# Kernel tuning notes

Measured on AMD Instinct MI355X. Metric: run time of the kernel, lower is better.

## Reference

```python
import jax, jax.numpy as jnp
import numpy as np

N_NODES = 50000
N_EDGES = 1600000
D = 128
L = 4
N_GRAPHS = 512


def setup_inputs() -> dict:
    key = jax.random.key(0)
    ks = jax.random.split(key, 8)
    x = jax.random.normal(ks[0], (N_NODES, D), dtype=jnp.float32)
    edge_index = jax.random.randint(ks[1], (2, N_EDGES), 0, N_NODES, dtype=jnp.int64)
    batch = jnp.sort(jax.random.randint(ks[2], (N_NODES,), 0, N_GRAPHS, dtype=jnp.int64))
    # MLP params per GIN layer: Linear(D->D), ReLU, Linear(D->D). Stacked over L layers.
    s = 1.0 / np.sqrt(D)
    Ws1 = jax.random.uniform(ks[3], (L, D, D), jnp.float32, -s, s)
    bs1 = jax.random.uniform(ks[4], (L, D), jnp.float32, -s, s)
    Ws2 = jax.random.uniform(ks[5], (L, D, D), jnp.float32, -s, s)
    bs2 = jax.random.uniform(ks[6], (L, D), jnp.float32, -s, s)
    return {"x": x, "edge_index": edge_index, "batch": batch,
            "Ws1": Ws1, "bs1": bs1, "Ws2": Ws2, "bs2": bs2}


def reference(x, edge_index, batch, Ws1, bs1, Ws2, bs2):
    src, dst = edge_index[0], edge_index[1]
    for l in range(L):
        # GINConv (eps=0): h = MLP(x + sum_{j in N(i)} x_j)
        agg = jax.ops.segment_sum(x[src], dst, num_segments=N_NODES)  # [N, D]
        h = x + agg
        h = jax.nn.relu(h @ Ws1[l] + bs1[l])
        x = h @ Ws2[l] + bs2[l]
    # global_add_pool: segment-sum node features by graph id
    return jax.ops.segment_sum(x, batch, num_segments=N_GRAPHS)  # [G, D]
```

## Files before the change

### kernel.cpp

```cpp
#include <hip/hip_runtime.h>

#define NN 50000
#define NE 1600000
#define DD 128
#define NL 4
#define NG 512
#define BSH 7
#define BMSK 127
#define NBUK 391
#define NBLK 196
#define EPB 8192
#define HN (NBUK * NBLK)
#define HT 150
#define EPT 20

typedef __attribute__((ext_vector_type(8))) short short8;
typedef __attribute__((ext_vector_type(4))) float floatx4;

__device__ __forceinline__ unsigned short f2bf(float f) {
    unsigned int u = __float_as_uint(f);
    u += 0x7fffu + ((u >> 16) & 1u);
    return (unsigned short)(u >> 16);
}
__device__ __forceinline__ float bf2f(unsigned short u) {
    return __uint_as_float(((unsigned int)u) << 16);
}

__global__ __launch_bounds__(256) void cvt_kernel(const float* __restrict__ x,
                                                  unsigned short* __restrict__ xbf) {
    int idx = blockIdx.x * 256 + threadIdx.x;
    float4 f = ((const float4*)x)[idx];
    ushort4 o;
    o.x = f2bf(f.x); o.y = f2bf(f.y); o.z = f2bf(f.z); o.w = f2bf(f.w);
    ((ushort4*)xbf)[idx] = o;
}


__global__ __launch_bounds__(512) void shist_kernel(const int* __restrict__ src,
                                                    int* __restrict__ hist) {
    __shared__ int h[NBUK];
    int tid = threadIdx.x;
    for (int i = tid; i < NBUK; i += 512) h[i] = 0;
    __syncthreads();
    int base = blockIdx.x * EPB;
#pragma unroll
    for (int it = 0; it < EPB / 512; it++) {
        int e = base + it * 512 + tid;
        if (e < NE) atomicAdd(&h[src[e] >> BSH], 1);
    }
    __syncthreads();
    for (int i = tid; i < NBUK; i += 512) hist[i * NBLK + blockIdx.x] = h[i];
}

__global__ __launch_bounds__(512) void sum_tiles_kernel(const int* __restrict__ in,
                                                        int* __restrict__ tsum, int n) {
    int i = blockIdx.x * 512 + threadIdx.x;
    __shared__ int s[512];
    s[threadIdx.x] = (i < n) ? in[i] : 0;
    __syncthreads();
    for (int off = 256; off > 0; off >>= 1) {
        if (threadIdx.x < off) s[threadIdx.x] += s[threadIdx.x + off];
        __syncthreads();
    }
    if (threadIdx.x == 0) tsum[blockIdx.x] = s[0];
}

__global__ __launch_bounds__(256) void scan_tiles_kernel(const int* __restrict__ tsum,
                                                         int* __restrict__ toff, int ntiles) {
    int t = threadIdx.x;
    __shared__ int s[256];
    int v = (t < ntiles) ? tsum[t] : 0;
    s[t] = v;
    __syncthreads();
    for (int off = 1; off < 256; off <<= 1) {
        int u = (t >= off) ? s[t - off] : 0;
        __syncthreads();
        s[t] += u;
        __syncthreads();
    }
    if (t < ntiles) toff[t] = s[t] - v;
}

__global__ __launch_bounds__(512) void scan_out_kernel(const int* __restrict__ in,
                                                       const int* __restrict__ toff,
                                                       int* __restrict__ out, int n) {
    int i = blockIdx.x * 512 + threadIdx.x;
    int t = threadIdx.x;
    int v = (i < n) ? in[i] : 0;
    __shared__ int s[512];
    s[t] = v;
    __syncthreads();
    for (int off = 1; off < 512; off <<= 1) {
        int u = (t >= off) ? s[t - off] : 0;
        __syncthreads();
        s[t] += u;
        __syncthreads();
    }
    if (i < n) out[i] = toff[blockIdx.x] + s[t] - v;
}

__global__ __launch_bounds__(512) void sscatter_kernel(const int* __restrict__ src,
                                                       const int* __restrict__ dst,
                                                       const int* __restrict__ soff,
                                                       unsigned int* __restrict__ ebufA) {
    __shared__ int h[NBUK];
    int tid = threadIdx.x;
    for (int i = tid; i < NBUK; i += 512) h[i] = 0;
    __syncthreads();
    int base = blockIdx.x * EPB;
#pragma unroll
    for (int it = 0; it < EPB / 512; it++) {
        int e = base + it * 512 + tid;
        if (e < NE) {
            int s = src[e];
            int ss = s >> BSH;
            int p = atomicAdd(&h[ss], 1);
            ebufA[soff[ss * NBLK + blockIdx.x] + p] =
                ((unsigned int)dst[e] << 16) | (unsigned int)s;
        }
    }
}

__global__ __launch_bounds__(512) void bhist_kernel(const unsigned int* __restrict__ ebufA,
                                                    int* __restrict__ hist) {
    __shared__ int h[NBUK];
    int tid = threadIdx.x;
    for (int i = tid; i < NBUK; i += 512) h[i] = 0;
    __syncthreads();
    int base = blockIdx.x * EPB;
#pragma unroll
    for (int it = 0; it < EPB / 512; it++) {
        int e = base + it * 512 + tid;
        if (e < NE) atomicAdd(&h[ebufA[e] >> (16 + BSH)], 1);
    }
    __syncthreads();
    for (int i = tid; i < NBUK; i += 512) hist[i * NBLK + blockIdx.x] = h[i];
}

__global__ __launch_bounds__(512) void bscatter_kernel(const unsigned int* __restrict__ ebufA,
                                                       const int* __restrict__ bkoff,
                                                       int* __restrict__ ebuf) {
    __shared__ int h[NBUK];
    int tid = threadIdx.x;
    for (int i = tid; i < NBUK; i += 512) h[i] = 0;
    __syncthreads();
    int base = blockIdx.x * EPB;
#pragma unroll
    for (int it = 0; it < EPB / 512; it++) {
        int e = base + it * 512 + tid;
        if (e < NE) {
            unsigned int pk = ebufA[e];
            int d = pk >> 16;
            int s = pk & 0xFFFF;
            int bu = d >> BSH;
            int p = atomicAdd(&h[bu], 1);
            ebuf[bkoff[bu * NBLK + blockIdx.x] + p] = (s << BSH) | (d & BMSK);
        }
    }
}

__global__ __launch_bounds__(256) void bucket_csr_kernel(const int* __restrict__ ebuf,
                                                         const int* __restrict__ bkoff,
                                                         int* __restrict__ rowptr,
                                                         int* __restrict__ rowend,
                                                         int* __restrict__ col) {
    __shared__ int cnt[128], exc[128], ebase[128];
    int b = blockIdx.x, tid = threadIdx.x;
    int segstart = bkoff[b * NBLK];
    int segend = (b < NBUK - 1) ? bkoff[(b + 1) * NBLK] : NE;
    if (tid < 128) cnt[tid] = 0;
    __syncthreads();
    int evr[EPT];
    int rnk[EPT];
#pragma unroll
    for (int j = 0; j < EPT; j++) {
        int i = segstart + tid + j * 256;
        if (i < segend) {
            int ev = ebuf[i];
            evr[j] = ev;
            rnk[j] = atomicAdd(&cnt[ev & BMSK], 1);
        } else {
            evr[j] = -1;
        }
    }
    __syncthreads();
    int v = (tid < 128) ? cnt[tid] : 0;
    if (tid < 128) exc[tid] = v;
    __syncthreads();
    for (int off = 1; off < 128; off <<= 1) {
        int u = (tid < 128 && tid >= off) ? exc[tid - off] : 0;
        __syncthreads();
        if (tid < 128) exc[tid] += u;
        __syncthreads();
    }
    if (tid < 128) {
        int excl = exc[tid] - v;
        ebase[tid] = segstart + excl;
        int node = (b << BSH) + tid;
        if (node < NN) {
            rowptr[node] = segstart + excl;
            rowend[node] = segstart + excl + v;
        }
    }
    __syncthreads();
#pragma unroll
    for (int j = 0; j < EPT; j++) {
        if (evr[j] >= 0) {
            int low = evr[j] & BMSK;
            col[ebase[low] + rnk[j]] = ((unsigned)evr[j]) >> BSH;
        }
    }
}

__global__ __launch_bounds__(256) void prep_kernel(const float* __restrict__ Ws1,
                                                   const float* __restrict__ Ws2,
                                                   unsigned short* __restrict__ W1T,
                                                   unsigned short* __restrict__ W2T) {
    int idx = blockIdx.x * 256 + threadIdx.x;
    int l = idx >> 14;
    int rem = idx & 16383;
    int k = rem >> 7;
    int n = rem & 127;
    int o = (l << 14) + (n << 7) + k;
    W1T[o] = f2bf(Ws1[idx]);
    W2T[o] = f2bf(Ws2[idx]);
}

__global__ __launch_bounds__(256) void agg_kernel(const unsigned short* __restrict__ xbf,
                                                  const int* __restrict__ rowptr,
                                                  const int* __restrict__ rowend,
                                                  const int* __restrict__ col,
                                                  unsigned short* __restrict__ hpre) {
    int g = threadIdx.x >> 4;
    int lane = threadIdx.x & 15;
    int node = blockIdx.x * 16 + g;
    const uint4* base = (const uint4*)xbf;
    float a[8];
    {
        uint4 v = base[node * 16 + lane];
        a[0] = __uint_as_float(v.x << 16); a[1] = __uint_as_float(v.x & 0xFFFF0000u);
        a[2] = __uint_as_float(v.y << 16); a[3] = __uint_as_float(v.y & 0xFFFF0000u);
        a[4] = __uint_as_float(v.z << 16); a[5] = __uint_as_float(v.z & 0xFFFF0000u);
        a[6] = __uint_as_float(v.w << 16); a[7] = __uint_as_float(v.w & 0xFFFF0000u);
    }
    int s = rowptr[node], e = rowend[node];
    int i = s;
    for (; i + 8 <= e; i += 8) {
        uint4 v0 = base[col[i] * 16 + lane];
        uint4 v1 = base[col[i + 1] * 16 + lane];
        uint4 v2 = base[col[i + 2] * 16 + lane];
        uint4 v3 = base[col[i + 3] * 16 + lane];
        uint4 v4 = base[col[i + 4] * 16 + lane];
        uint4 v5 = base[col[i + 5] * 16 + lane];
        uint4 v6 = base[col[i + 6] * 16 + lane];
        uint4 v7 = base[col[i + 7] * 16 + lane];
#define ACC(V)                                                            \
        a[0] += __uint_as_float(V.x << 16); a[1] += __uint_as_float(V.x & 0xFFFF0000u); \
        a[2] += __uint_as_float(V.y << 16); a[3] += __uint_as_float(V.y & 0xFFFF0000u); \
        a[4] += __uint_as_float(V.z << 16); a[5] += __uint_as_float(V.z & 0xFFFF0000u); \
        a[6] += __uint_as_float(V.w << 16); a[7] += __uint_as_float(V.w & 0xFFFF0000u)
        ACC(v0); ACC(v1); ACC(v2); ACC(v3); ACC(v4); ACC(v5); ACC(v6); ACC(v7);
    }
    for (; i < e; i++) {
        uint4 v = base[col[i] * 16 + lane];
        ACC(v);
    }
#undef ACC
    uint4 o;
    o.x = (unsigned int)f2bf(a[0]) | ((unsigned int)f2bf(a[1]) << 16);
    o.y = (unsigned int)f2bf(a[2]) | ((unsigned int)f2bf(a[3]) << 16);
    o.z = (unsigned int)f2bf(a[4]) | ((unsigned int)f2bf(a[5]) << 16);
    o.w = (unsigned int)f2bf(a[6]) | ((unsigned int)f2bf(a[7]) << 16);
    ((uint4*)hpre)[node * 16 + lane] = o;
}

__global__ __launch_bounds__(256) void mlp_kernel(const unsigned short* __restrict__ A,
                                                  const unsigned short* __restrict__ W1,
                                                  const float* __restrict__ b1,
                                                  const unsigned short* __restrict__ W2,
                                                  const float* __restrict__ b2,
                                                  unsigned short* __restrict__ O) {
    __shared__ unsigned short Wl[128 * 128];
    __shared__ unsigned short Hl[128 * 128];
    int tid = threadIdx.x;
    int wg = tid >> 6;
    int lane = tid & 63;
    int quad = lane >> 4;
    int li = lane & 15;
    int mg = wg >> 1, ng = wg & 1;
    int rowb = blockIdx.x * 128;

    {
        const uint4* wgl = (const uint4*)W1;
#pragma unroll
        for (int it = 0; it < 8; it++) {
            int idx = it * 256 + tid;
            int n = idx >> 4, kc = idx & 15;
            *(uint4*)&Wl[n * 128 + ((kc * 8) ^ ((n & 7) << 3))] = wgl[idx];
        }
    }
    __syncthreads();

    floatx4 acc[4][4];
#pragma unroll
    for (int tn = 0; tn < 4; tn++)
#pragma unroll
        for (int mi = 0; mi < 4; mi++) acc[tn][mi] = (floatx4){0.f, 0.f, 0.f, 0.f};

#pragma unroll
    for (int kk = 0; kk < 4; kk++) {
        int kc = kk * 32 + quad * 8;
        short8 xf[4];
#pragma unroll
        for (int mi = 0; mi < 4; mi++) {
            int ar = rowb + mg * 64 + mi * 16 + li;
            xf[mi] = (ar < NN) ? *(const short8*)(A + (size_t)ar * DD + kc)
                               : (short8){0, 0, 0, 0, 0, 0, 0, 0};
        }
#pragma unroll
        for (int tn = 0; tn < 4; tn++) {
            int wr = ng * 64 + tn * 16 + li;
            short8 wf = *(const short8*)&Wl[wr * 128 + (kc ^ ((wr & 7) << 3))];
#pragma unroll
            for (int mi = 0; mi < 4; mi++)
                acc[tn][mi] = __builtin_amdgcn_mfma_f32_16x16x32_bf16(wf, xf[mi], acc[tn][mi], 0, 0, 0);
        }
    }

#pragma unroll
    for (int tn = 0; tn < 4; tn++) {
        float4 bv = ((const float4*)b1)[ng * 16 + tn * 4 + quad];
#pragma unroll
        for (int mi = 0; mi < 4; mi++) {
            int hr = mg * 64 + mi * 16 + li;
            float v0 = fmaxf(acc[tn][mi][0] + bv.x, 0.f);
            float v1 = fmaxf(acc[tn][mi][1] + bv.y, 0.f);
            float v2 = fmaxf(acc[tn][mi][2] + bv.z, 0.f);
            float v3 = fmaxf(acc[tn][mi][3] + bv.w, 0.f);
            uint2 u;
            u.x = (unsigned int)f2bf(v0) | ((unsigned int)f2bf(v1) << 16);
            u.y = (unsigned int)f2bf(v2) | ((unsigned int)f2bf(v3) << 16);
            int c = (ng * 64 + tn * 16 + quad * 4) ^ ((hr & 7) << 3);
            *(uint2*)&Hl[hr * 128 + c] = u;
        }
    }
    __syncthreads();

    {
        const uint4* wgl = (const uint4*)W2;
#pragma unroll
        for (int it = 0; it < 8; it++) {
            int idx = it * 256 + tid;
            int n = idx >> 4, kc = idx & 15;
            *(uint4*)&Wl[n * 128 + ((kc * 8) ^ ((n & 7) << 3))] = wgl[idx];
        }
    }
    __syncthreads();

#pragma unroll
    for (int tn = 0; tn < 4; tn++)
#pragma unroll
        for (int mi = 0; mi < 4; mi++) acc[tn][mi] = (floatx4){0.f, 0.f, 0.f, 0.f};

#pragma unroll
    for (int kk = 0; kk < 4; kk++) {
        int kc = kk * 32 + quad * 8;
        short8 hf[4];
#pragma unroll
        for (int mi = 0; mi < 4; mi++) {
            int hr = mg * 64 + mi * 16 + li;
            hf[mi] = *(const short8*)&Hl[hr * 128 + (kc ^ ((hr & 7) << 3))];
        }
#pragma unroll
        for (int tn = 0; tn < 4; tn++) {
            int wr = ng * 64 + tn * 16 + li;
            short8 wf = *(const short8*)&Wl[wr * 128 + (kc ^ ((wr & 7) << 3))];
#pragma unroll
            for (int mi = 0; mi < 4; mi++)
                acc[tn][mi] = __builtin_amdgcn_mfma_f32_16x16x32_bf16(wf, hf[mi], acc[tn][mi], 0, 0, 0);
        }
    }

#pragma unroll
    for (int tn = 0; tn < 4; tn++) {
        float4 bv = ((const float4*)b2)[ng * 16 + tn * 4 + quad];
#pragma unroll
        for (int mi = 0; mi < 4; mi++) {
            int m = rowb + mg * 64 + mi * 16 + li;
            if (m < NN) {
                uint2 u;
                u.x = (unsigned int)f2bf(acc[tn][mi][0] + bv.x) |
                      ((unsigned int)f2bf(acc[tn][mi][1] + bv.y) << 16);
                u.y = (unsigned int)f2bf(acc[tn][mi][2] + bv.z) |
                      ((unsigned int)f2bf(acc[tn][mi][3] + bv.w) << 16);
                *(uint2*)&O[(size_t)m * DD + ng * 64 + tn * 16 + quad * 4] = u;
            }
        }
    }
}

__global__ __launch_bounds__(128) void pool_kernel(const unsigned short* __restrict__ x,
                                                   const int* __restrict__ batch,
                                                   float* __restrict__ out) {
    int g = blockIdx.x;
    int lo = 0, hi = NN;
    while (lo < hi) { int mid = (lo + hi) >> 1; if (batch[mid] < g) lo = mid + 1; else hi = mid; }
    int s = lo;
    hi = NN;
    while (lo < hi) { int mid = (lo + hi) >> 1; if (batch[mid] < g + 1) lo = mid + 1; else hi = mid; }
    int e = lo;
    int d = threadIdx.x;
    float acc = 0.f;
    for (int i = s; i < e; i++) acc += bf2f(x[(size_t)i * DD + d]);
    out[g * DD + d] = acc;
}

extern "C" void kernel_launch(void* const* d_in, const int* in_sizes, int n_in,
                              void* d_out, int out_size, void* d_ws, size_t ws_size,
                              hipStream_t stream) {
    const float* x0 = (const float*)d_in[0];
    const int* edge = (const int*)d_in[1];
    const int* batch = (const int*)d_in[2];
    const float* Ws1 = (const float*)d_in[3];
    const float* bs1 = (const float*)d_in[4];
    const float* Ws2 = (const float*)d_in[5];
    const float* bs2 = (const float*)d_in[6];
    float* out = (float*)d_out;
    const int* src = edge;
    const int* dst = edge + NE;

    char* ws = (char*)d_ws;
    size_t off = 0;
    auto alloc = [&](size_t bytes) {
        void* p = ws + off;
        off += (bytes + 255) & ~(size_t)255;
        return p;
    };
    unsigned short* x0bf = (unsigned short*)alloc((size_t)NN * DD * 2);
    unsigned short* xA = (unsigned short*)alloc((size_t)NN * DD * 2);
    unsigned short* xB = (unsigned short*)alloc((size_t)NN * DD * 2);
    unsigned short* hpre = (unsigned short*)alloc((size_t)NN * DD * 2);
    int* col = (int*)alloc((size_t)NE * 4);
    int* ebuf = (int*)alloc((size_t)NE * 4);
    unsigned int* ebufA = (unsigned int*)alloc((size_t)NE * 4);
    int* hist = (int*)alloc((size_t)HN * 4);
    int* bkoff = (int*)alloc((size_t)HN * 4);
    int* soff = (int*)alloc((size_t)HN * 4);
    int* tsum = (int*)alloc((size_t)HT * 4);
    int* toff = (int*)alloc((size_t)HT * 4);
    int* rowptr = (int*)alloc((size_t)(NN + 1) * 4);
    int* rowend = (int*)alloc((size_t)NN * 4);
    unsigned short* W1T = (unsigned short*)alloc((size_t)NL * DD * DD * 2);
    unsigned short* W2T = (unsigned short*)alloc((size_t)NL * DD * DD * 2);

    cvt_kernel<<<(NN * DD / 4) / 256, 256, 0, stream>>>(x0, x0bf);
    shist_kernel<<<NBLK, 512, 0, stream>>>(src, hist);
    sum_tiles_kernel<<<HT, 512, 0, stream>>>(hist, tsum, HN);
    scan_tiles_kernel<<<1, 256, 0, stream>>>(tsum, toff, HT);
    scan_out_kernel<<<HT, 512, 0, stream>>>(hist, toff, soff, HN);
    sscatter_kernel<<<NBLK, 512, 0, stream>>>(src, dst, soff, ebufA);
    bhist_kernel<<<NBLK, 512, 0, stream>>>(ebufA, hist);
    sum_tiles_kernel<<<HT, 512, 0, stream>>>(hist, tsum, HN);
    scan_tiles_kernel<<<1, 256, 0, stream>>>(tsum, toff, HT);
    scan_out_kernel<<<HT, 512, 0, stream>>>(hist, toff, bkoff, HN);
    bscatter_kernel<<<NBLK, 512, 0, stream>>>(ebufA, bkoff, ebuf);
    bucket_csr_kernel<<<NBUK, 256, 0, stream>>>(ebuf, bkoff, rowptr, rowend, col);
    prep_kernel<<<(NL * DD * DD) / 256, 256, 0, stream>>>(Ws1, Ws2, W1T, W2T);

    const unsigned short* xin = x0bf;
    unsigned short* bufs[2] = {xA, xB};
    const int mlp_grid = (NN + 127) / 128;
    for (int l = 0; l < NL; l++) {
        agg_kernel<<<NN / 16, 256, 0, stream>>>(xin, rowptr, rowend, col, hpre);
        unsigned short* xout = bufs[l & 1];
        mlp_kernel<<<mlp_grid, 256, 0, stream>>>(hpre, W1T + l * DD * DD, bs1 + l * DD,
                                                 W2T + l * DD * DD, bs2 + l * DD, xout);
        xin = xout;
    }
    pool_kernel<<<NG, 128, 0, stream>>>(xin, batch, out);
}
```

Measured before the change: 453.3 us.

## Fuse prelude kernels and replace three-pass scan with single-pass lookback scan

Merges the x conversion, weight transpose/convert and source histogram into one prelude kernel. Replaces each three-kernel scan (tile sums, tile scan, output scan) with a single-pass decoupled-lookback scan that uses per-tile status flags in global memory, which are reset by a memset. This cuts kernel launches and inter-kernel gaps in the CSR build. The lookback spin-waits rely on all 150 blocks being co-resident, and the memset adds one extra operation.

```diff
diff --git a/kernel.cpp b/kernel.cpp
--- a/kernel.cpp
+++ b/kernel.cpp
@@ -13,6 +13,8 @@
 #define HN (NBUK * NBLK)
 #define HT 150
 #define EPT 20
+#define CVT_N (NN * DD / 4)
+#define PREP_N (NL * DD * DD)
 
 typedef __attribute__((ext_vector_type(8))) short short8;
 typedef __attribute__((ext_vector_type(4))) float floatx4;
@@ -26,78 +28,81 @@
     return __uint_as_float(((unsigned int)u) << 16);
 }
 
-__global__ __launch_bounds__(256) void cvt_kernel(const float* __restrict__ x,
-                                                  unsigned short* __restrict__ xbf) {
-    int idx = blockIdx.x * 256 + threadIdx.x;
-    float4 f = ((const float4*)x)[idx];
-    ushort4 o;
-    o.x = f2bf(f.x); o.y = f2bf(f.y); o.z = f2bf(f.z); o.w = f2bf(f.w);
-    ((ushort4*)xbf)[idx] = o;
-}
-
-
-__global__ __launch_bounds__(512) void shist_kernel(const int* __restrict__ src,
-                                                    int* __restrict__ hist) {
+__global__ __launch_bounds__(512) void prelude_kernel(
+    const float* __restrict__ x0, const float* __restrict__ Ws1,
+    const float* __restrict__ Ws2, const int* __restrict__ src,
+    unsigned short* __restrict__ xbf, unsigned short* __restrict__ W1T,
+    unsigned short* __restrict__ W2T, int* __restrict__ hist) {
     __shared__ int h[NBUK];
-    int tid = threadIdx.x;
+    int tid = threadIdx.x, bid = blockIdx.x;
+    int gid = bid * 512 + tid;
+    for (int idx = gid; idx < CVT_N; idx += NBLK * 512) {
+        float4 f = ((const float4*)x0)[idx];
+        ushort4 o;
+        o.x = f2bf(f.x); o.y = f2bf(f.y); o.z = f2bf(f.z); o.w = f2bf(f.w);
+        ((ushort4*)xbf)[idx] = o;
+    }
+    for (int idx = gid; idx < PREP_N; idx += NBLK * 512) {
+        int l = idx >> 14, rem = idx & 16383;
+        int k = rem >> 7, n = rem & 127;
+        int o = (l << 14) + (n << 7) + k;
+        W1T[o] = f2bf(Ws1[idx]);
+        W2T[o] = f2bf(Ws2[idx]);
+    }
     for (int i = tid; i < NBUK; i += 512) h[i] = 0;
     __syncthreads();
-    int base = blockIdx.x * EPB;
-#pragma unroll
-    for (int it = 0; it < EPB / 512; it++) {
-        int e = base + it * 512 + tid;
-        if (e < NE) atomicAdd(&h[src[e] >> BSH], 1);
-    }
-    __syncthreads();
-    for (int i = tid; i < NBUK; i += 512) hist[i * NBLK + blockIdx.x] = h[i];
-}
-
-__global__ __launch_bounds__(512) void sum_tiles_kernel(const int* __restrict__ in,
-                                                        int* __restrict__ tsum, int n) {
-    int i = blockIdx.x * 512 + threadIdx.x;
+    {
+        int base = bid * EPB;
+        int end = base + EPB; if (end > NE) end = NE;
+        for (int e = base + tid; e < end; e += 512) atomicAdd(&h[src[e] >> BSH], 1);
+    }
+    __syncthreads();
+    for (int i = tid; i < NBUK; i += 512) hist[i * NBLK + bid] = h[i];
+}
+
+__global__ __launch_bounds__(512) void scan_lb_kernel(const int* __restrict__ in,
+                                                      int* __restrict__ out,
+                                                      unsigned int* __restrict__ tstat,
+                                                      int n) {
     __shared__ int s[512];
-    s[threadIdx.x] = (i < n) ? in[i] : 0;
+    int b = blockIdx.x, tid = threadIdx.x;
+    int i = b * 512 + tid;
+    int v = (i < n) ? in[i] : 0;
+    s[tid] = v;
+    __syncthreads();
+    for (int off = 1; off < 512; off <<= 1) {
+        int u = (tid >= off) ? s[tid - off] : 0;
+        __syncthreads();
+        s[tid] += u;
+        __syncthreads();
+    }
+    int incl = s[tid];
+    int agg = s[511];
+    if (tid == 0)
+        __hip_atomic_store(&tstat[b], 0x80000000u | (unsigned int)agg,
+                           __ATOMIC_RELAXED, __HIP_MEMORY_SCOPE_AGENT);
+    unsigned int got = 0;
+    if (tid < b) {
+        unsigned int x = __hip_atomic_load(&tstat[tid], __ATOMIC_RELAXED,
+                                           __HIP_MEMORY_SCOPE_AGENT);
+        while (!(x & 0x80000000u)) {
+            __builtin_amdgcn_s_sleep(1);
+            x = __hip_atomic_load(&tstat[tid], __ATOMIC_RELAXED,
+                                  __HIP_MEMORY_SCOPE_AGENT);
+        }
+        got = x & 0x7FFFFFFFu;
+    }
+    __syncthreads();
+    s[tid] = (int)got;
     __syncthreads();
     for (int off = 256; off > 0; off >>= 1) {
-        if (threadIdx.x < off) s[threadIdx.x] += s[threadIdx.x + off];
+        if (tid < off) s[tid] += s[tid + off];
         __syncthreads();
     }
-    if (threadIdx.x == 0) tsum[blockIdx.x] = s[0];
-}
-
-__global__ __launch_bounds__(256) void scan_tiles_kernel(const int* __restrict__ tsum,
-                                                         int* __restrict__ toff, int ntiles) {
-    int t = threadIdx.x;
-    __shared__ int s[256];
-    int v = (t < ntiles) ? tsum[t] : 0;
-    s[t] = v;
-    __syncthreads();
-    for (int off = 1; off < 256; off <<= 1) {
-        int u = (t >= off) ? s[t - off] : 0;
-        __syncthreads();
-        s[t] += u;
-        __syncthreads();
-    }
-    if (t < ntiles) toff[t] = s[t] - v;
-}
-
-__global__ __launch_bounds__(512) void scan_out_kernel(const int* __restrict__ in,
-                                                       const int* __restrict__ toff,
-                                                       int* __restrict__ out, int n) {
-    int i = blockIdx.x * 512 + threadIdx.x;
-    int t = threadIdx.x;
-    int v = (i < n) ? in[i] : 0;
-    __shared__ int s[512];
-    s[t] = v;
-    __syncthreads();
-    for (int off = 1; off < 512; off <<= 1) {
-        int u = (t >= off) ? s[t - off] : 0;
-        __syncthreads();
-        s[t] += u;
-        __syncthreads();
-    }
-    if (i < n) out[i] = toff[blockIdx.x] + s[t] - v;
-}
+    int carry = s[0];
+    if (i < n) out[i] = carry + incl - v;
+}
+
 
 __global__ __launch_bounds__(512) void sscatter_kernel(const int* __restrict__ src,
                                                        const int* __restrict__ dst,
@@ -210,20 +215,6 @@
             col[ebase[low] + rnk[j]] = ((unsigned)evr[j]) >> BSH;
         }
     }
-}
-
-__global__ __launch_bounds__(256) void prep_kernel(const float* __restrict__ Ws1,
-                                                   const float* __restrict__ Ws2,
-                                                   unsigned short* __restrict__ W1T,
-                                                   unsigned short* __restrict__ W2T) {
-    int idx = blockIdx.x * 256 + threadIdx.x;
-    int l = idx >> 14;
-    int rem = idx & 16383;
-    int k = rem >> 7;
-    int n = rem & 127;
-    int o = (l << 14) + (n << 7) + k;
-    W1T[o] = f2bf(Ws1[idx]);
-    W2T[o] = f2bf(Ws2[idx]);
 }
 
 __global__ __launch_bounds__(256) void agg_kernel(const unsigned short* __restrict__ xbf,
@@ -446,26 +437,22 @@
     int* hist = (int*)alloc((size_t)HN * 4);
     int* bkoff = (int*)alloc((size_t)HN * 4);
     int* soff = (int*)alloc((size_t)HN * 4);
-    int* tsum = (int*)alloc((size_t)HT * 4);
-    int* toff = (int*)alloc((size_t)HT * 4);
     int* rowptr = (int*)alloc((size_t)(NN + 1) * 4);
     int* rowend = (int*)alloc((size_t)NN * 4);
     unsigned short* W1T = (unsigned short*)alloc((size_t)NL * DD * DD * 2);
     unsigned short* W2T = (unsigned short*)alloc((size_t)NL * DD * DD * 2);
-
-    cvt_kernel<<<(NN * DD / 4) / 256, 256, 0, stream>>>(x0, x0bf);
-    shist_kernel<<<NBLK, 512, 0, stream>>>(src, hist);
-    sum_tiles_kernel<<<HT, 512, 0, stream>>>(hist, tsum, HN);
-    scan_tiles_kernel<<<1, 256, 0, stream>>>(tsum, toff, HT);
-    scan_out_kernel<<<HT, 512, 0, stream>>>(hist, toff, soff, HN);
+    unsigned int* tstat = (unsigned int*)alloc(4096);
+    unsigned int* tstatA = tstat;
+    unsigned int* tstatB = tstat + 512;
+
+    (void)hipMemsetAsync(tstat, 0, 4096, stream);
+    prelude_kernel<<<NBLK, 512, 0, stream>>>(x0, Ws1, Ws2, src, x0bf, W1T, W2T, hist);
+    scan_lb_kernel<<<HT, 512, 0, stream>>>(hist, soff, tstatA, HN);
     sscatter_kernel<<<NBLK, 512, 0, stream>>>(src, dst, soff, ebufA);
     bhist_kernel<<<NBLK, 512, 0, stream>>>(ebufA, hist);
-    sum_tiles_kernel<<<HT, 512, 0, stream>>>(hist, tsum, HN);
-    scan_tiles_kernel<<<1, 256, 0, stream>>>(tsum, toff, HT);
-    scan_out_kernel<<<HT, 512, 0, stream>>>(hist, toff, bkoff, HN);
+    scan_lb_kernel<<<HT, 512, 0, stream>>>(hist, bkoff, tstatB, HN);
     bscatter_kernel<<<NBLK, 512, 0, stream>>>(ebufA, bkoff, ebuf);
     bucket_csr_kernel<<<NBUK, 256, 0, stream>>>(ebuf, bkoff, rowptr, rowend, col);
-    prep_kernel<<<(NL * DD * DD) / 256, 256, 0, stream>>>(Ws1, Ws2, W1T, W2T);
 
     const unsigned short* xin = x0bf;
     unsigned short* bufs[2] = {xA, xB};
```

Result: no change. 449.4 us (-0.9%).
